# Kernel optimization log

Measured on AMD Instinct MI355X. Metric: run time of the kernel, lower is better.

The kernel has to match this reference:

```python
import jax, jax.numpy as jnp
import numpy as np

N_NODES = 100000
IN_F = 512
OUT_F = 512
N_EDGES = 3200000


def setup_inputs() -> dict:
    key = jax.random.key(0)
    k1, k2, k3, k4, k5 = jax.random.split(key, 5)
    features = jax.random.normal(k1, (N_NODES, IN_F), dtype=jnp.float32)
    # xavier_uniform: bound = sqrt(6/(in+out))
    bound = np.sqrt(6.0 / (IN_F + OUT_F)).astype(np.float32)
    weight = jax.random.uniform(k2, (IN_F, OUT_F), dtype=jnp.float32,
                                minval=-bound, maxval=bound)
    edge_row = jax.random.randint(k3, (N_EDGES,), 0, N_NODES, dtype=jnp.int32)
    edge_col = jax.random.randint(k4, (N_EDGES,), 0, N_NODES, dtype=jnp.int32)
    # normalized-adjacency-like positive values
    edge_val = jax.random.uniform(k5, (N_EDGES,), dtype=jnp.float32)
    return {"features": features, "weight": weight, "edge_row": edge_row,
            "edge_col": edge_col, "edge_val": edge_val}


def reference(features, weight, edge_row, edge_col, edge_val):
    # support = features @ W   (dense GEMM, [N, out])
    support = features @ weight
    # output = spmm(adj, support): out[r] += val * support[c] for each edge (r, c)
    messages = edge_val[:, None] * support[edge_col]          # [E, out]
    output = jax.ops.segment_sum(messages, edge_row, num_segments=N_NODES)
    # active=True branch: fused ReLU
    return jax.nn.relu(output)
```

## Files before the change

### kernel.cpp

```cpp
#include <hip/hip_runtime.h>
#include <hip/hip_bf16.h>

#define N_NODES 100000
#define M_PAD   100096
#define FDIM    512
#define N_EDGES 3200000
#define GEMM_BLOCKS 3128
#define GEMM_MAIN   3104

#define NB    391
#define B1    782
#define SLICE 4096

typedef __attribute__((ext_vector_type(8))) short short8;
typedef __attribute__((ext_vector_type(8))) unsigned short ushort8;
typedef __attribute__((ext_vector_type(4))) unsigned short ushort4_t;
typedef __attribute__((ext_vector_type(4))) float floatx4;
typedef __attribute__((ext_vector_type(2))) int intx2;

__device__ __forceinline__ unsigned short f2bf(float f) {
    unsigned u = __float_as_uint(f);
    u += 0x7FFFu + ((u >> 16) & 1u);
    return (unsigned short)(u >> 16);
}
__device__ __forceinline__ float bf2f(unsigned short u) {
    return __uint_as_float(((unsigned)u) << 16);
}

__global__ __launch_bounds__(256) void convert_w_k(const float* __restrict__ W,
                                                   unsigned short* __restrict__ Wt) {
    int idx = blockIdx.x * 256 + threadIdx.x;
    int k = idx >> 9, n = idx & 511;
    Wt[n * 512 + k] = f2bf(W[idx]);
}

__global__ __launch_bounds__(256) void convert_a_k(const float* __restrict__ F,
                                                   unsigned short* __restrict__ Af) {
    int i = blockIdx.x * 256 + threadIdx.x;
    if (i >= (N_NODES * FDIM) / 8) return;
    const float4* p = (const float4*)F + (size_t)i * 2;
    float4 a = p[0], b = p[1];
    ushort8 u = { f2bf(a.x), f2bf(a.y), f2bf(a.z), f2bf(a.w),
                  f2bf(b.x), f2bf(b.y), f2bf(b.z), f2bf(b.w) };
    *(ushort8*)(Af + (size_t)i * 8) = u;
}

__global__ __launch_bounds__(256) void hist1_k(const int* __restrict__ row,
                                               int* __restrict__ H) {
    __shared__ int h[NB];
    const int b = blockIdx.x;
    for (int k = threadIdx.x; k < NB; k += 256) h[k] = 0;
    __syncthreads();
    const int base = b * SLICE;
    const int limit = min(base + SLICE, N_EDGES);
    for (int i = base + threadIdx.x; i < limit; i += 256)
        atomicAdd(&h[row[i] >> 8], 1);
    __syncthreads();
    for (int k = threadIdx.x; k < NB; k += 256)
        H[b * NB + k] = h[k];
}

__global__ __launch_bounds__(1024) void scanA_k(int* __restrict__ H,
                                                int* __restrict__ totals) {
    __shared__ int sm[1024];
    const int k = blockIdx.x, tid = threadIdx.x;
    int v = (tid < B1) ? H[tid * NB + k] : 0;
    sm[tid] = v;
    __syncthreads();
    #pragma unroll
    for (int off = 1; off < 1024; off <<= 1) {
        int t = (tid >= off) ? sm[tid - off] : 0;
        __syncthreads();
        sm[tid] += t;
        __syncthreads();
    }
    if (tid < B1) H[tid * NB + k] = sm[tid] - v;
    if (tid == B1 - 1) totals[k] = sm[tid];
}

__global__ __launch_bounds__(512) void scanB_k(const int* __restrict__ totals,
                                               int* __restrict__ start) {
    __shared__ int sm[512];
    const int tid = threadIdx.x;
    int v = (tid < NB) ? totals[tid] : 0;
    sm[tid] = v;
    __syncthreads();
    #pragma unroll
    for (int off = 1; off < 512; off <<= 1) {
        int t = (tid >= off) ? sm[tid - off] : 0;
        __syncthreads();
        sm[tid] += t;
        __syncthreads();
    }
    if (tid < NB) start[tid] = sm[tid] - v;
    if (tid == 0) start[NB] = N_EDGES;
}

__global__ __launch_bounds__(256) void scatter1_k(const int* __restrict__ row,
                                                  const int* __restrict__ col,
                                                  const float* __restrict__ val,
                                                  const int* __restrict__ H,
                                                  const int* __restrict__ start,
                                                  int2* __restrict__ tmp_cv,
                                                  unsigned char* __restrict__ tmp_r8) {
    __shared__ int cur[NB];
    const int b = blockIdx.x;
    for (int k = threadIdx.x; k < NB; k += 256)
        cur[k] = start[k] + H[b * NB + k];
    __syncthreads();
    const int base = b * SLICE;
    const int limit = min(base + SLICE, N_EDGES);
    for (int i = base + threadIdx.x; i < limit; i += 256) {
        int r = row[i];
        int p = atomicAdd(&cur[r >> 8], 1);
        tmp_cv[p] = make_int2(col[i], __float_as_int(val[i]));
        tmp_r8[p] = (unsigned char)(r & 255);
    }
}

__global__ __launch_bounds__(256) void sort2_k(const int* __restrict__ start,
                                               const int2* __restrict__ tmp_cv,
                                               const unsigned char* __restrict__ tmp_r8,
                                               int* __restrict__ row_start,
                                               int2* __restrict__ edges) {
    __shared__ int h[256];
    __shared__ int cur[256];
    const int k = blockIdx.x, tid = threadIdx.x;
    const int base = start[k], cnt = start[k + 1] - base;
    h[tid] = 0;
    __syncthreads();
    for (int i = tid; i < cnt; i += 256)
        atomicAdd(&h[tmp_r8[base + i]], 1);
    __syncthreads();
    int v = h[tid];
    #pragma unroll
    for (int off = 1; off < 256; off <<= 1) {
        int t = (tid >= off) ? h[tid - off] : 0;
        __syncthreads();
        h[tid] += t;
        __syncthreads();
    }
    int excl = h[tid] - v;
    int r = (k << 8) + tid;
    if (r < N_NODES) row_start[r] = base + excl;
    cur[tid] = base + excl;
    if (k == NB - 1 && tid == 0) row_start[N_NODES] = N_EDGES;
    __syncthreads();
    for (int i = tid; i < cnt; i += 256) {
        unsigned char rl = tmp_r8[base + i];
        int p = atomicAdd(&cur[rl], 1);
        edges[p] = tmp_cv[base + i];
    }
}

__global__ __launch_bounds__(256) void gemm_k(const unsigned short* __restrict__ A,
                                              const unsigned short* __restrict__ Bt,
                                              unsigned short* __restrict__ C) {
    const int id = blockIdx.x;
    int mb, nb;
    if (id < GEMM_MAIN) {
        mb = (id >> 5) * 8 + (id & 7);
        nb = (id >> 3) & 3;
    } else {
        int t = id - GEMM_MAIN;
        mb = 776 + (t >> 2);
        nb = t & 3;
    }
    const int baseM = mb * 128;
    const int baseN = nb * 128;
    const int tid  = threadIdx.x;
    const int lane = tid & 63, wave = tid >> 6;
    const int wm = (wave & 1) * 64;
    const int wn = (wave >> 1) * 64;
    const int lrow = lane & 15, quad = lane >> 4;

    __shared__ unsigned short As[128 * 32];
    __shared__ unsigned short Bs[128 * 32];

    floatx4 acc[4][4] = {};

    for (int k0 = 0; k0 < FDIM; k0 += 32) {
        #pragma unroll
        for (int i = 0; i < 2; ++i) {
            int ofs = i * 4096 + tid * 16;
            int row = ofs >> 6;
            int ke  = (ofs & 63) >> 1;
            __builtin_amdgcn_global_load_lds(
                (const __attribute__((address_space(1))) void*)
                    (A + (size_t)(baseM + row) * FDIM + k0 + ke),
                (__attribute__((address_space(3))) void*)((char*)As + ofs),
                16, 0, 0);
            __builtin_amdgcn_global_load_lds(
                (const __attribute__((address_space(1))) void*)
                    (Bt + (size_t)(baseN + row) * FDIM + k0 + ke),
                (__attribute__((address_space(3))) void*)((char*)Bs + ofs),
                16, 0, 0);
        }
        __syncthreads();

        short8 af[4], bfr[4];
        #pragma unroll
        for (int mi = 0; mi < 4; ++mi)
            af[mi] = *(const short8*)(As + (wm + mi * 16 + lrow) * 32 + quad * 8);
        #pragma unroll
        for (int ni = 0; ni < 4; ++ni)
            bfr[ni] = *(const short8*)(Bs + (wn + ni * 16 + lrow) * 32 + quad * 8);
        #pragma unroll
        for (int mi = 0; mi < 4; ++mi)
            #pragma unroll
            for (int ni = 0; ni < 4; ++ni)
                acc[mi][ni] = __builtin_amdgcn_mfma_f32_16x16x32_bf16(
                    af[mi], bfr[ni], acc[mi][ni], 0, 0, 0);
        __syncthreads();
    }

    #pragma unroll
    for (int mi = 0; mi < 4; ++mi)
        #pragma unroll
        for (int ni = 0; ni < 4; ++ni)
            #pragma unroll
            for (int rr = 0; rr < 4; ++rr) {
                int row  = baseM + wm + mi * 16 + quad * 4 + rr;
                int colj = baseN + wn + ni * 16 + lrow;
                if (row < N_NODES)
                    C[(size_t)row * FDIM + colj] = f2bf(acc[mi][ni][rr]);
            }
}

__global__ __launch_bounds__(64) void spmm_k(const unsigned short* __restrict__ sup,
                                             const int* __restrict__ row_start,
                                             const int2* __restrict__ edges,
                                             float* __restrict__ out) {
    const int r = blockIdx.x;
    const int lane = threadIdx.x;
    const int start = row_start[r], end = row_start[r + 1];
    const unsigned short* supl = sup + lane * 8;

    float acc[8] = {0.f, 0.f, 0.f, 0.f, 0.f, 0.f, 0.f, 0.f};

    const int n8 = (end - start) & ~7;
    for (int eb = start; eb < start + n8; eb += 8) {
        intx2 p[8];
        #pragma unroll
        for (int j = 0; j < 8; ++j)
            p[j] = __builtin_nontemporal_load((const intx2*)&edges[eb + j]);
        ushort8 s[8];
        #pragma unroll
        for (int j = 0; j < 8; ++j)
            s[j] = *(const ushort8*)(supl + (size_t)p[j].x * FDIM);
        #pragma unroll
        for (int j = 0; j < 8; ++j) {
            float v = __int_as_float(p[j].y);
            #pragma unroll
            for (int i = 0; i < 8; ++i)
                acc[i] += v * bf2f((unsigned short)s[j][i]);
        }
    }
    for (int e = start + n8; e < end; ++e) {
        intx2 p = __builtin_nontemporal_load((const intx2*)&edges[e]);
        ushort8 s = *(const ushort8*)(supl + (size_t)p.x * FDIM);
        float v = __int_as_float(p.y);
        #pragma unroll
        for (int i = 0; i < 8; ++i) acc[i] += v * bf2f((unsigned short)s[i]);
    }

    float* op = out + (size_t)r * FDIM + lane * 8;
    floatx4 o0 = { fmaxf(acc[0], 0.f), fmaxf(acc[1], 0.f),
                   fmaxf(acc[2], 0.f), fmaxf(acc[3], 0.f) };
    floatx4 o1 = { fmaxf(acc[4], 0.f), fmaxf(acc[5], 0.f),
                   fmaxf(acc[6], 0.f), fmaxf(acc[7], 0.f) };
    __builtin_nontemporal_store(o0, (floatx4*)op);
    __builtin_nontemporal_store(o1, (floatx4*)(op + 4));
}

extern "C" void kernel_launch(void* const* d_in, const int* in_sizes, int n_in,
                              void* d_out, int out_size, void* d_ws, size_t ws_size,
                              hipStream_t stream) {
    const float* features = (const float*)d_in[0];
    const float* weight   = (const float*)d_in[1];
    const int*   edge_row = (const int*)d_in[2];
    const int*   edge_col = (const int*)d_in[3];
    const float* edge_val = (const float*)d_in[4];
    float* out = (float*)d_out;

    char* ws = (char*)d_ws;
    size_t off = 0;
    unsigned short* sup = (unsigned short*)(ws + off); off += (size_t)N_NODES * FDIM * 2;
    unsigned short* Af  = (unsigned short*)(ws + off); off += (size_t)M_PAD * FDIM * 2;
    unsigned short* Wt  = (unsigned short*)(ws + off); off += (size_t)FDIM * FDIM * 2;
    int* row_start = (int*)(ws + off); off += 400128;
    int2* edges    = (int2*)(ws + off); off += (size_t)N_EDGES * 8;
    char* supb = (char*)sup;
    int2* tmp_cv         = (int2*)(supb);
    unsigned char* tmp_r8 = (unsigned char*)(supb + 25600000);
    int* H      = (int*)(supb + 28800000);
    int* totals = (int*)(supb + 30026240);
    int* startb = (int*)(supb + 30030336);

    convert_w_k<<<dim3((FDIM * FDIM) / 256), dim3(256), 0, stream>>>(weight, Wt);
    convert_a_k<<<dim3((N_NODES * FDIM / 8 + 255) / 256), dim3(256), 0, stream>>>(features, Af);
    hist1_k<<<dim3(B1), dim3(256), 0, stream>>>(edge_row, H);
    scanA_k<<<dim3(NB), dim3(1024), 0, stream>>>(H, totals);
    scanB_k<<<dim3(1), dim3(512), 0, stream>>>(totals, startb);
    scatter1_k<<<dim3(B1), dim3(256), 0, stream>>>(edge_row, edge_col, edge_val,
                                                   H, startb, tmp_cv, tmp_r8);
    sort2_k<<<dim3(NB), dim3(256), 0, stream>>>(startb, tmp_cv, tmp_r8, row_start, edges);
    gemm_k<<<dim3(GEMM_BLOCKS), dim3(256), 0, stream>>>(Af, Wt, sup);
    spmm_k<<<dim3(N_NODES), dim3(64), 0, stream>>>(sup, row_start, edges, out);
}
```

Measured before the change: 1.082 ms.

## Use finer row buckets, deeper GEMM K-tile, and 4-row SpMM blocks

The radix bucketing of edges by row now uses 128-row buckets (782 buckets) instead of 256-row ones, so the second-pass sort blocks and scans are smaller and there are more of them. The GEMM K-step is doubled to 64, which halves the number of barrier pairs per tile at the cost of twice the LDS per block. The SpMM kernel packs four rows per 256-thread block instead of launching one 64-thread block per row, which cuts block-launch overhead. The workspace offsets for the histogram totals are shifted to fit the larger histogram.

```diff
diff --git a/kernel.cpp b/kernel.cpp
--- a/kernel.cpp
+++ b/kernel.cpp
@@ -8,13 +8,12 @@
 #define GEMM_BLOCKS 3128
 #define GEMM_MAIN   3104
 
-#define NB    391
+#define NB    782
 #define B1    782
 #define SLICE 4096
 
 typedef __attribute__((ext_vector_type(8))) short short8;
 typedef __attribute__((ext_vector_type(8))) unsigned short ushort8;
-typedef __attribute__((ext_vector_type(4))) unsigned short ushort4_t;
 typedef __attribute__((ext_vector_type(4))) float floatx4;
 typedef __attribute__((ext_vector_type(2))) int intx2;
 
@@ -54,7 +53,7 @@
     const int base = b * SLICE;
     const int limit = min(base + SLICE, N_EDGES);
     for (int i = base + threadIdx.x; i < limit; i += 256)
-        atomicAdd(&h[row[i] >> 8], 1);
+        atomicAdd(&h[row[i] >> 7], 1);
     __syncthreads();
     for (int k = threadIdx.x; k < NB; k += 256)
         H[b * NB + k] = h[k];
@@ -78,15 +77,15 @@
     if (tid == B1 - 1) totals[k] = sm[tid];
 }
 
-__global__ __launch_bounds__(512) void scanB_k(const int* __restrict__ totals,
-                                               int* __restrict__ start) {
-    __shared__ int sm[512];
+__global__ __launch_bounds__(1024) void scanB_k(const int* __restrict__ totals,
+                                                int* __restrict__ start) {
+    __shared__ int sm[1024];
     const int tid = threadIdx.x;
     int v = (tid < NB) ? totals[tid] : 0;
     sm[tid] = v;
     __syncthreads();
     #pragma unroll
-    for (int off = 1; off < 512; off <<= 1) {
+    for (int off = 1; off < 1024; off <<= 1) {
         int t = (tid >= off) ? sm[tid - off] : 0;
         __syncthreads();
         sm[tid] += t;
@@ -112,9 +111,9 @@
     const int limit = min(base + SLICE, N_EDGES);
     for (int i = base + threadIdx.x; i < limit; i += 256) {
         int r = row[i];
-        int p = atomicAdd(&cur[r >> 8], 1);
+        int p = atomicAdd(&cur[r >> 7], 1);
         tmp_cv[p] = make_int2(col[i], __float_as_int(val[i]));
-        tmp_r8[p] = (unsigned char)(r & 255);
+        tmp_r8[p] = (unsigned char)(r & 127);
     }
 }
 
@@ -123,27 +122,29 @@
                                                const unsigned char* __restrict__ tmp_r8,
                                                int* __restrict__ row_start,
                                                int2* __restrict__ edges) {
-    __shared__ int h[256];
-    __shared__ int cur[256];
+    __shared__ int h[128];
+    __shared__ int cur[128];
     const int k = blockIdx.x, tid = threadIdx.x;
     const int base = start[k], cnt = start[k + 1] - base;
-    h[tid] = 0;
+    if (tid < 128) h[tid] = 0;
     __syncthreads();
     for (int i = tid; i < cnt; i += 256)
         atomicAdd(&h[tmp_r8[base + i]], 1);
     __syncthreads();
-    int v = h[tid];
+    int v = (tid < 128) ? h[tid] : 0;
     #pragma unroll
-    for (int off = 1; off < 256; off <<= 1) {
-        int t = (tid >= off) ? h[tid - off] : 0;
-        __syncthreads();
-        h[tid] += t;
-        __syncthreads();
-    }
-    int excl = h[tid] - v;
-    int r = (k << 8) + tid;
-    if (r < N_NODES) row_start[r] = base + excl;
-    cur[tid] = base + excl;
+    for (int off = 1; off < 128; off <<= 1) {
+        int t = (tid >= off && tid < 128) ? h[tid - off] : 0;
+        __syncthreads();
+        if (tid < 128) h[tid] += t;
+        __syncthreads();
+    }
+    if (tid < 128) {
+        int excl = h[tid] - v;
+        int r = (k << 7) + tid;
+        if (r < N_NODES) row_start[r] = base + excl;
+        cur[tid] = base + excl;
+    }
     if (k == NB - 1 && tid == 0) row_start[N_NODES] = N_EDGES;
     __syncthreads();
     for (int i = tid; i < cnt; i += 256) {
@@ -174,17 +175,17 @@
     const int wn = (wave >> 1) * 64;
     const int lrow = lane & 15, quad = lane >> 4;
 
-    __shared__ unsigned short As[128 * 32];
-    __shared__ unsigned short Bs[128 * 32];
+    __shared__ unsigned short As[128 * 64];
+    __shared__ unsigned short Bs[128 * 64];
 
     floatx4 acc[4][4] = {};
 
-    for (int k0 = 0; k0 < FDIM; k0 += 32) {
-        #pragma unroll
-        for (int i = 0; i < 2; ++i) {
+    for (int k0 = 0; k0 < FDIM; k0 += 64) {
+        #pragma unroll
+        for (int i = 0; i < 4; ++i) {
             int ofs = i * 4096 + tid * 16;
-            int row = ofs >> 6;
-            int ke  = (ofs & 63) >> 1;
+            int row = ofs >> 7;
+            int ke  = (ofs & 127) >> 1;
             __builtin_amdgcn_global_load_lds(
                 (const __attribute__((address_space(1))) void*)
                     (A + (size_t)(baseM + row) * FDIM + k0 + ke),
@@ -198,19 +199,25 @@
         }
         __syncthreads();
 
-        short8 af[4], bfr[4];
+        short8 af[4][2], bfr[4][2];
         #pragma unroll
         for (int mi = 0; mi < 4; ++mi)
-            af[mi] = *(const short8*)(As + (wm + mi * 16 + lrow) * 32 + quad * 8);
+            #pragma unroll
+            for (int kk = 0; kk < 2; ++kk)
+                af[mi][kk] = *(const short8*)(As + (wm + mi * 16 + lrow) * 64 + kk * 32 + quad * 8);
         #pragma unroll
         for (int ni = 0; ni < 4; ++ni)
-            bfr[ni] = *(const short8*)(Bs + (wn + ni * 16 + lrow) * 32 + quad * 8);
-        #pragma unroll
-        for (int mi = 0; mi < 4; ++mi)
-            #pragma unroll
-            for (int ni = 0; ni < 4; ++ni)
-                acc[mi][ni] = __builtin_amdgcn_mfma_f32_16x16x32_bf16(
-                    af[mi], bfr[ni], acc[mi][ni], 0, 0, 0);
+            #pragma unroll
+            for (int kk = 0; kk < 2; ++kk)
+                bfr[ni][kk] = *(const short8*)(Bs + (wn + ni * 16 + lrow) * 64 + kk * 32 + quad * 8);
+        #pragma unroll
+        for (int kk = 0; kk < 2; ++kk)
+            #pragma unroll
+            for (int mi = 0; mi < 4; ++mi)
+                #pragma unroll
+                for (int ni = 0; ni < 4; ++ni)
+                    acc[mi][ni] = __builtin_amdgcn_mfma_f32_16x16x32_bf16(
+                        af[mi][kk], bfr[ni][kk], acc[mi][ni], 0, 0, 0);
         __syncthreads();
     }
 
@@ -227,12 +234,12 @@
             }
 }
 
-__global__ __launch_bounds__(64) void spmm_k(const unsigned short* __restrict__ sup,
-                                             const int* __restrict__ row_start,
-                                             const int2* __restrict__ edges,
-                                             float* __restrict__ out) {
-    const int r = blockIdx.x;
-    const int lane = threadIdx.x;
+__global__ __launch_bounds__(256) void spmm_k(const unsigned short* __restrict__ sup,
+                                              const int* __restrict__ row_start,
+                                              const int2* __restrict__ edges,
+                                              float* __restrict__ out) {
+    const int r = blockIdx.x * 4 + (threadIdx.x >> 6);
+    const int lane = threadIdx.x & 63;
     const int start = row_start[r], end = row_start[r + 1];
     const unsigned short* supl = sup + lane * 8;
 
@@ -291,20 +298,20 @@
     int* row_start = (int*)(ws + off); off += 400128;
     int2* edges    = (int2*)(ws + off); off += (size_t)N_EDGES * 8;
     char* supb = (char*)sup;
-    int2* tmp_cv         = (int2*)(supb);
+    int2* tmp_cv          = (int2*)(supb);
     unsigned char* tmp_r8 = (unsigned char*)(supb + 25600000);
     int* H      = (int*)(supb + 28800000);
-    int* totals = (int*)(supb + 30026240);
-    int* startb = (int*)(supb + 30030336);
+    int* totals = (int*)(supb + 31246336);
+    int* startb = (int*)(supb + 31250432);
 
     convert_w_k<<<dim3((FDIM * FDIM) / 256), dim3(256), 0, stream>>>(weight, Wt);
     convert_a_k<<<dim3((N_NODES * FDIM / 8 + 255) / 256), dim3(256), 0, stream>>>(features, Af);
     hist1_k<<<dim3(B1), dim3(256), 0, stream>>>(edge_row, H);
     scanA_k<<<dim3(NB), dim3(1024), 0, stream>>>(H, totals);
-    scanB_k<<<dim3(1), dim3(512), 0, stream>>>(totals, startb);
+    scanB_k<<<dim3(1), dim3(1024), 0, stream>>>(totals, startb);
     scatter1_k<<<dim3(B1), dim3(256), 0, stream>>>(edge_row, edge_col, edge_val,
                                                    H, startb, tmp_cv, tmp_r8);
     sort2_k<<<dim3(NB), dim3(256), 0, stream>>>(startb, tmp_cv, tmp_r8, row_start, edges);
     gemm_k<<<dim3(GEMM_BLOCKS), dim3(256), 0, stream>>>(Af, Wt, sup);
-    spmm_k<<<dim3(N_NODES), dim3(64), 0, stream>>>(sup, row_start, edges, out);
-}
+    spmm_k<<<dim3(N_NODES / 4), dim3(256), 0, stream>>>(sup, row_start, edges, out);
+}
```

Result: no change. 1.101 ms (+1.7%).
